# Kernel optimization log

Hardware: AMD Instinct MI355X
Metric: run time of the kernel (lower is better)

Reference implementation:

```python
import jax, jax.numpy as jnp
import numpy as np

B, C, H, W = 2, 64, 128, 128

def setup_inputs() -> dict:
    key = jax.random.key(0)
    k1, k2, k3 = jax.random.split(key, 3)
    x = jax.random.normal(k1, (B, C, H, W), dtype=jnp.float32)
    y = jax.random.normal(k2, (B, C, H, W), dtype=jnp.float32)
    z = jax.random.normal(k3, (B, C, H, W), dtype=jnp.float32)
    return {"x": x, "y": y, "z": z}

def reference(x, y, z):
    # x=q, y=k, z=v, all [b,c,h,w]. Per pixel:
    #   kv[i,j] = v[i] * k[j]          (c x c outer product)
    #   attn    = softmax over i (dim=1 in torch, the v axis)
    #   out[i]  = sum_j attn[i,j] * q[j]
    q = jnp.transpose(x, (0, 2, 3, 1))  # [b,h,w,c]
    k = jnp.transpose(y, (0, 2, 3, 1))
    v = jnp.transpose(z, (0, 2, 3, 1))
    kv = v[..., :, None] * k[..., None, :]          # [b,h,w,c,c]
    attn = jax.nn.softmax(kv, axis=-2)              # softmax over v-axis i
    out = jnp.einsum('bhwij,bhwj->bhwi', attn, q)   # [b,h,w,c]
    return jnp.transpose(out, (0, 3, 1, 2))         # [b,c,h,w]
```

## Files before the change

kernel.cpp:

```cpp
#include <hip/hip_runtime.h>


constexpr int C    = 64;
constexpr int HW   = 128 * 128;
constexpr int NPIX = 2 * HW;
constexpr int ICH  = 8;
#define LOG2E 1.4426950408889634f

__device__ __forceinline__ float quad_xor1_add(float x) {
  int xi = __builtin_bit_cast(int, x);
  int yi = __builtin_amdgcn_update_dpp(0, xi, 0xB1, 0xF, 0xF, true);
  return x + __builtin_bit_cast(float, yi);
}
__device__ __forceinline__ float quad_xor2_add(float x) {
  int xi = __builtin_bit_cast(int, x);
  int yi = __builtin_amdgcn_update_dpp(0, xi, 0x4E, 0xF, 0xF, true);
  return x + __builtin_bit_cast(float, yi);
}
__device__ __forceinline__ float xor4_add(float x) {
  int xi = __builtin_bit_cast(int, x);
  int yi = __builtin_amdgcn_ds_swizzle(xi, 0x101F);
  return x + __builtin_bit_cast(float, yi);
}

__global__ __launch_bounds__(256) void channel_mixing_kernel(
    const float* __restrict__ q,
    const float* __restrict__ kk,
    const float* __restrict__ v,
    float* __restrict__ out) {
  const int lane = threadIdx.x & 63;
  const int wave = blockIdx.x * 4 + (threadIdx.x >> 6);
  const int p    = lane >> 3;
  const int ig   = lane & 7;
  const int pix  = wave * 8 + p;

  const int base  = ((pix >> 14) << 20) | (pix & (HW - 1));
  const int cbase = base + (ig << 17);

  float vv[ICH];
#pragma unroll
  for (int ii = 0; ii < ICH; ++ii)
    vv[ii] = v[cbase + (ii << 14)] * LOG2E;

  float acc[ICH];
#pragma unroll
  for (int ii = 0; ii < ICH; ++ii) acc[ii] = 0.0f;

#pragma unroll 8
  for (int j = 0; j < C; ++j) {
    const float kj = kk[base + (j << 14)];
    const float qj = q[base + (j << 14)];

    float e[ICH];
#pragma unroll
    for (int ii = 0; ii < ICH; ++ii)
      e[ii] = __builtin_amdgcn_exp2f(vv[ii] * kj);

    float s0 = (e[0] + e[1]) + (e[2] + e[3]);
    float s1 = (e[4] + e[5]) + (e[6] + e[7]);
    float S  = s0 + s1;
    S = quad_xor1_add(S);
    S = quad_xor2_add(S);
    S = xor4_add(S);

    const float w = qj * __builtin_amdgcn_rcpf(S);
#pragma unroll
    for (int ii = 0; ii < ICH; ++ii) acc[ii] += w * e[ii];
  }

#pragma unroll
  for (int ii = 0; ii < ICH; ++ii)
    out[cbase + (ii << 14)] = acc[ii];
}

extern "C" void kernel_launch(void* const* d_in, const int* in_sizes, int n_in,
                              void* d_out, int out_size, void* d_ws, size_t ws_size,
                              hipStream_t stream) {
  const float* q  = (const float*)d_in[0];
  const float* kk = (const float*)d_in[1];
  const float* v  = (const float*)d_in[2];
  float* out = (float*)d_out;

  dim3 grid(NPIX / 32);
  dim3 block(256);
  channel_mixing_kernel<<<grid, block, 0, stream>>>(q, kk, v, out);
}
```

Before: 103.9 us.

## Stage k and q per block in LDS and batch cross-lane reductions

Each block now cooperatively loads the k and q channel vectors for its 32 pixels into padded shared memory. Previously 8 lanes per pixel each issued redundant global loads for every channel. The inner loop then processes 8 channels at a time, reading them as float4 from LDS and interleaving the DPP/swizzle reductions so the shuffles can overlap. This adds a barrier, 17KB of LDS per block, more live registers under a 4-blocks occupancy hint, and some spill risk.

```diff
diff --git a/kernel.cpp b/kernel.cpp
--- a/kernel.cpp
+++ b/kernel.cpp
@@ -5,6 +5,8 @@
 constexpr int HW   = 128 * 128;
 constexpr int NPIX = 2 * HW;
 constexpr int ICH  = 8;
+constexpr int JT   = 8;
+constexpr int LSTR = 68;
 #define LOG2E 1.4426950408889634f
 
 __device__ __forceinline__ float quad_xor1_add(float x) {
@@ -23,18 +25,32 @@
   return x + __builtin_bit_cast(float, yi);
 }
 
-__global__ __launch_bounds__(256) void channel_mixing_kernel(
+__global__ __launch_bounds__(256, 4) void channel_mixing_kernel(
     const float* __restrict__ q,
     const float* __restrict__ kk,
     const float* __restrict__ v,
     float* __restrict__ out) {
-  const int lane = threadIdx.x & 63;
-  const int wave = blockIdx.x * 4 + (threadIdx.x >> 6);
+  __shared__ __align__(16) float lds_k[32 * LSTR];
+  __shared__ __align__(16) float lds_q[32 * LSTR];
+
+  const int t        = threadIdx.x;
+  const int pixblock = blockIdx.x * 32;
+  const int gbase = ((pixblock >> 14) << 20) | (pixblock & (HW - 1));
+
+#pragma unroll
+  for (int rep = 0; rep < 8; ++rep) {
+    const int idx = rep * 256 + t;
+    const int j   = idx >> 5;
+    const int px  = idx & 31;
+    lds_k[px * LSTR + j] = kk[gbase + (j << 14) + px];
+    lds_q[px * LSTR + j] = q [gbase + (j << 14) + px];
+  }
+
+  const int lane = t & 63;
   const int p    = lane >> 3;
   const int ig   = lane & 7;
-  const int pix  = wave * 8 + p;
-
-  const int base  = ((pix >> 14) << 20) | (pix & (HW - 1));
+  const int px   = (t >> 6) * 8 + p;
+  const int base  = gbase + px;
   const int cbase = base + (ig << 17);
 
   float vv[ICH];
@@ -46,26 +62,46 @@
 #pragma unroll
   for (int ii = 0; ii < ICH; ++ii) acc[ii] = 0.0f;
 
-#pragma unroll 8
-  for (int j = 0; j < C; ++j) {
-    const float kj = kk[base + (j << 14)];
-    const float qj = q[base + (j << 14)];
+  __syncthreads();
 
-    float e[ICH];
+  const float* lkp = &lds_k[px * LSTR];
+  const float* lqp = &lds_q[px * LSTR];
+
+#pragma unroll 1
+  for (int jt = 0; jt < C / JT; ++jt) {
+    float kx[JT], qx[JT];
+    *(float4*)&kx[0] = *(const float4*)&lkp[jt * JT];
+    *(float4*)&kx[4] = *(const float4*)&lkp[jt * JT + 4];
+    *(float4*)&qx[0] = *(const float4*)&lqp[jt * JT];
+    *(float4*)&qx[4] = *(const float4*)&lqp[jt * JT + 4];
+
+    float e[JT][ICH];
 #pragma unroll
-    for (int ii = 0; ii < ICH; ++ii)
-      e[ii] = __builtin_amdgcn_exp2f(vv[ii] * kj);
+    for (int jj = 0; jj < JT; ++jj)
+#pragma unroll
+      for (int ii = 0; ii < ICH; ++ii)
+        e[jj][ii] = __builtin_amdgcn_exp2f(vv[ii] * kx[jj]);
 
-    float s0 = (e[0] + e[1]) + (e[2] + e[3]);
-    float s1 = (e[4] + e[5]) + (e[6] + e[7]);
-    float S  = s0 + s1;
-    S = quad_xor1_add(S);
-    S = quad_xor2_add(S);
-    S = xor4_add(S);
+    float S[JT];
+#pragma unroll
+    for (int jj = 0; jj < JT; ++jj) {
+      float s0 = (e[jj][0] + e[jj][1]) + (e[jj][2] + e[jj][3]);
+      float s1 = (e[jj][4] + e[jj][5]) + (e[jj][6] + e[jj][7]);
+      S[jj] = s0 + s1;
+    }
+#pragma unroll
+    for (int jj = 0; jj < JT; ++jj) S[jj] = quad_xor1_add(S[jj]);
+#pragma unroll
+    for (int jj = 0; jj < JT; ++jj) S[jj] = quad_xor2_add(S[jj]);
+#pragma unroll
+    for (int jj = 0; jj < JT; ++jj) S[jj] = xor4_add(S[jj]);
 
-    const float w = qj * __builtin_amdgcn_rcpf(S);
 #pragma unroll
-    for (int ii = 0; ii < ICH; ++ii) acc[ii] += w * e[ii];
+    for (int jj = 0; jj < JT; ++jj) {
+      const float w = qx[jj] * __builtin_amdgcn_rcpf(S[jj]);
+#pragma unroll
+      for (int ii = 0; ii < ICH; ++ii) acc[ii] += w * e[jj][ii];
+    }
   }
 
 #pragma unroll
```

New measurement: 92.90 us. -10.6%, faster.
